# Kernel tuning notes

Measured on AMD Instinct MI355X. Metric: run time of the kernel, lower is better.

## Reference

```python
import jax, jax.numpy as jnp
import numpy as np

CONSOLIDATION_RATE = 0.001
FORGETTING_RATE = 0.0001
INITIAL_CONSOLIDATION_TIME = 100
WEIGHT_DIM = (4096, 4096)


def setup_inputs() -> dict:
    key = jax.random.key(0)
    ks = jax.random.split(key, 8)
    return {
        "current_weights": jax.random.normal(ks[0], WEIGHT_DIM, dtype=jnp.float32) * 0.1,
        "weight_changes": jax.random.normal(ks[1], WEIGHT_DIM, dtype=jnp.float32) * 0.01,
        # update_rule: Linear(3,16) -> ReLU -> Linear(16,1) -> Tanh
        "ur_w1": jax.random.normal(ks[2], (16, 3), dtype=jnp.float32) * 0.5,
        "ur_b1": jnp.zeros((16,), dtype=jnp.float32),
        "ur_w2": jax.random.normal(ks[3], (1, 16), dtype=jnp.float32) * 0.3,
        "ur_b2": jnp.zeros((1,), dtype=jnp.float32),
        # forgetting_gater: Linear(2,8) -> ReLU -> Linear(8,1) -> Sigmoid
        "fg_w1": jax.random.normal(ks[4], (8, 2), dtype=jnp.float32) * 0.5,
        "fg_b1": jnp.zeros((8,), dtype=jnp.float32),
        "fg_w2": jax.random.normal(ks[5], (1, 8), dtype=jnp.float32) * 0.3,
        "fg_b2": jnp.zeros((1,), dtype=jnp.float32),
    }


def reference(current_weights, weight_changes, ur_w1, ur_b1, ur_w2, ur_b2,
              fg_w1, fg_b1, fg_w2, fg_b2):
    # --- consolidation strength (first call: history len == 1, so strength = base) ---
    base_strength = jax.nn.sigmoid(jnp.linalg.norm(current_weights))
    final_strength = jnp.clip(base_strength, 0.0, 1.0)
    change_magnitude = jnp.linalg.norm(weight_changes)  # reported only

    # --- forgetting gate: input [time_factor, forgetting_rate] ---
    time_factor = min(1.0 / INITIAL_CONSOLIDATION_TIME, 1.0)  # 0.01 (python const)
    fx = jnp.array([time_factor, FORGETTING_RATE], dtype=current_weights.dtype)
    fh = jax.nn.relu(fx @ fg_w1.T + fg_b1)                 # [8]
    forgetting_strength = jax.nn.sigmoid(fh @ fg_w2.T + fg_b2)[0]  # scalar

    # --- consolidation dynamics: tiny 3->16->1 MLP vectorized over all N elements ---
    flat = current_weights.reshape(-1)                      # [N]
    # inputs per element are (w_i, final_strength, forgetting_strength); the last two
    # are scalars, so fold them into a per-hidden-unit bias instead of building [N,3].
    hidden_bias = final_strength * ur_w1[:, 1] + forgetting_strength * ur_w1[:, 2] + ur_b1  # [16]
    h = jax.nn.relu(flat[:, None] * ur_w1[:, 0] + hidden_bias)  # [N,16]
    update = jnp.tanh(h @ ur_w2[0] + ur_b2[0]) * CONSOLIDATION_RATE  # [N]
    new_weights = jnp.clip(flat + update, -10.0, 10.0).reshape(current_weights.shape)

    # --- quality / stability / memory strength (first-call values) ---
    weight_stability = jnp.asarray(0.5, dtype=current_weights.dtype)  # history < 10
    mean_abs = jnp.mean(jnp.abs(new_weights))
    dist_quality = jnp.where((mean_abs > 0.1) & (mean_abs < 0.9), 1.0, mean_abs)
    consolidation_quality = (weight_stability + dist_quality) / 2.0
    memory_strength = jnp.asarray(0.0, dtype=current_weights.dtype)   # history < 5

    return (new_weights, final_strength, change_magnitude, forgetting_strength,
            consolidation_quality, weight_stability, memory_strength)
```

## Files before the change

### kernel.cpp

```cpp
#include <hip/hip_runtime.h>
#include <math.h>

typedef float vfloat4 __attribute__((ext_vector_type(4)));
typedef float vfloat2 __attribute__((ext_vector_type(2)));

#define UNROLL 8
#define NBLK 2048
#define THREADS 256


__global__ __launch_bounds__(256) void wc_reduce_w(const vfloat4* __restrict__ w,
                                                   float* __restrict__ w_part,
                                                   int n4) {
    int tid = blockIdx.x * blockDim.x + threadIdx.x;
    int stride = gridDim.x * blockDim.x;
    float s0 = 0.f, s1 = 0.f, s2 = 0.f, s3 = 0.f;
    int i = tid;
    for (; i + (UNROLL - 1) * stride < n4; i += UNROLL * stride) {
        vfloat4 a[UNROLL];
#pragma unroll
        for (int u = 0; u < UNROLL; u++) a[u] = w[i + u * stride];
#pragma unroll
        for (int u = 0; u < UNROLL; u++) {
            s0 = fmaf(a[u].x, a[u].x, s0);
            s1 = fmaf(a[u].y, a[u].y, s1);
            s2 = fmaf(a[u].z, a[u].z, s2);
            s3 = fmaf(a[u].w, a[u].w, s3);
        }
    }
    for (; i < n4; i += stride) {
        vfloat4 a = w[i];
        s0 = fmaf(a.x, a.x, s0); s1 = fmaf(a.y, a.y, s1);
        s2 = fmaf(a.z, a.z, s2); s3 = fmaf(a.w, a.w, s3);
    }
    float sw = (s0 + s1) + (s2 + s3);
    for (int off = 32; off > 0; off >>= 1) sw += __shfl_down(sw, off);
    __shared__ float ls[4];
    int wave = threadIdx.x >> 6;
    int lane = threadIdx.x & 63;
    if (lane == 0) ls[wave] = sw;
    __syncthreads();
    if (threadIdx.x == 0)
        w_part[blockIdx.x] = (ls[0] + ls[1]) + (ls[2] + ls[3]);
}

__global__ __launch_bounds__(1024) void wc_scalars(const float* __restrict__ w_part,
                                                   float* __restrict__ wsf,
                                                   const float* __restrict__ fg_w1,
                                                   const float* __restrict__ fg_b1,
                                                   const float* __restrict__ fg_w2,
                                                   const float* __restrict__ fg_b2,
                                                   float* __restrict__ out_tail) {
    double sw = 0.0;
    for (int i = threadIdx.x; i < NBLK; i += 1024) sw += (double)w_part[i];
    for (int off = 32; off > 0; off >>= 1) sw += __shfl_down(sw, off);
    __shared__ double lsw[16];
    int wave = threadIdx.x >> 6;
    int lane = threadIdx.x & 63;
    if (lane == 0) lsw[wave] = sw;
    __syncthreads();
    if (threadIdx.x == 0) {
        double tw = 0.0;
        for (int k = 0; k < 16; k++) tw += lsw[k];
        float normw = sqrtf((float)tw);
        float fs = 1.0f / (1.0f + expf(-normw));
        fs = fminf(fmaxf(fs, 0.0f), 1.0f);
        const float tf = 0.01f, fr = 0.0001f;
        float acc = fg_b2[0];
        for (int j = 0; j < 8; j++) {
            float h = tf * fg_w1[2 * j + 0] + fr * fg_w1[2 * j + 1] + fg_b1[j];
            acc = fmaf(fmaxf(h, 0.0f), fg_w2[j], acc);
        }
        float fg = 1.0f / (1.0f + expf(-acc));
        wsf[0] = fs;
        wsf[1] = fg;
        out_tail[0] = fs;
        out_tail[2] = fg;
        out_tail[4] = 0.5f;
        out_tail[5] = 0.0f;
    }
}

__global__ __launch_bounds__(256) void wc_consolidate(const vfloat4* __restrict__ w,
                                                      const vfloat4* __restrict__ dw,
                                                      vfloat4* __restrict__ outw,
                                                      const float* __restrict__ ur_w1,
                                                      const float* __restrict__ ur_b1,
                                                      const float* __restrict__ ur_w2,
                                                      const float* __restrict__ ur_b2,
                                                      const float* __restrict__ wsf,
                                                      vfloat2* __restrict__ cd_part,
                                                      int n4) {
    float fs = wsf[0];
    float fg = wsf[1];
    float a0[16], hb[16], w2[16];
#pragma unroll
    for (int k = 0; k < 16; k++) {
        a0[k] = ur_w1[3 * k + 0];
        hb[k] = fmaf(fs, ur_w1[3 * k + 1], fmaf(fg, ur_w1[3 * k + 2], ur_b1[k]));
        w2[k] = ur_w2[k];
    }
    float b2 = ur_b2[0];

    int tid = blockIdx.x * blockDim.x + threadIdx.x;
    int stride = gridDim.x * blockDim.x;
    float sabs = 0.f;
    vfloat2 sdv01 = {0.f, 0.f}, sdv23 = {0.f, 0.f};
    int i = tid;
    for (; i + (UNROLL - 1) * stride < n4; i += UNROLL * stride) {
        vfloat4 v[UNROLL], d[UNROLL];
#pragma unroll
        for (int u = 0; u < UNROLL; u++) v[u] = w[i + u * stride];
#pragma unroll
        for (int u = 0; u < UNROLL; u++) d[u] = dw[i + u * stride];
#pragma unroll
        for (int u = 0; u < UNROLL; u++) {
            vfloat2 d01 = {d[u].x, d[u].y}, d23 = {d[u].z, d[u].w};
            sdv01 += d01 * d01;
            sdv23 += d23 * d23;
            vfloat2 x01 = {v[u].x, v[u].y}, x23 = {v[u].z, v[u].w};
            vfloat2 acc01 = {b2, b2}, acc23 = {b2, b2};
#pragma unroll
            for (int k = 0; k < 16; k++) {
                vfloat2 h01 = x01 * a0[k] + hb[k];
                vfloat2 h23 = x23 * a0[k] + hb[k];
                h01 = __builtin_elementwise_max(h01, (vfloat2)0.0f);
                h23 = __builtin_elementwise_max(h23, (vfloat2)0.0f);
                acc01 += h01 * w2[k];
                acc23 += h23 * w2[k];
            }
            float accs[4] = {acc01.x, acc01.y, acc23.x, acc23.y};
            float xs[4] = {v[u].x, v[u].y, v[u].z, v[u].w};
            vfloat4 o;
#pragma unroll
            for (int e = 0; e < 4; e++) {
                float t = __expf(2.0f * accs[e]);
                float th = fmaf(-2.0f, __builtin_amdgcn_rcpf(t + 1.0f), 1.0f);
                float nw = fmaf(0.001f, th, xs[e]);
                nw = fminf(fmaxf(nw, -10.0f), 10.0f);
                o[e] = nw;
                sabs += fabsf(nw);
            }
            outw[i + u * stride] = o;
        }
    }
    for (; i < n4; i += stride) {
        vfloat4 v = w[i];
        vfloat4 d = dw[i];
        vfloat2 d01 = {d.x, d.y}, d23 = {d.z, d.w};
        sdv01 += d01 * d01;
        sdv23 += d23 * d23;
        vfloat4 o;
#pragma unroll
        for (int e = 0; e < 4; e++) {
            float x = v[e];
            float acc = b2;
#pragma unroll
            for (int k = 0; k < 16; k++) {
                float h = fmaf(x, a0[k], hb[k]);
                acc = fmaf(fmaxf(h, 0.0f), w2[k], acc);
            }
            float t = __expf(2.0f * acc);
            float th = fmaf(-2.0f, __builtin_amdgcn_rcpf(t + 1.0f), 1.0f);
            float nw = fmaf(0.001f, th, x);
            nw = fminf(fmaxf(nw, -10.0f), 10.0f);
            o[e] = nw;
            sabs += fabsf(nw);
        }
        outw[i] = o;
    }
    float sdw = (sdv01.x + sdv01.y) + (sdv23.x + sdv23.y);
    for (int off = 32; off > 0; off >>= 1) {
        sabs += __shfl_down(sabs, off);
        sdw  += __shfl_down(sdw, off);
    }
    __shared__ float lsa[4], lsd[4];
    int wave = threadIdx.x >> 6;
    int lane = threadIdx.x & 63;
    if (lane == 0) { lsa[wave] = sabs; lsd[wave] = sdw; }
    __syncthreads();
    if (threadIdx.x == 0) {
        vfloat2 p;
        p.x = (lsa[0] + lsa[1]) + (lsa[2] + lsa[3]);
        p.y = (lsd[0] + lsd[1]) + (lsd[2] + lsd[3]);
        cd_part[blockIdx.x] = p;
    }
}

__global__ __launch_bounds__(1024) void wc_finalize(const vfloat2* __restrict__ cd_part,
                                                    float* __restrict__ out_tail,
                                                    double inv_n) {
    double sa = 0.0, sd = 0.0;
    for (int i = threadIdx.x; i < NBLK; i += 1024) {
        vfloat2 p = cd_part[i];
        sa += (double)p.x;
        sd += (double)p.y;
    }
    for (int off = 32; off > 0; off >>= 1) {
        sa += __shfl_down(sa, off);
        sd += __shfl_down(sd, off);
    }
    __shared__ double lsa[16], lsd[16];
    int wave = threadIdx.x >> 6;
    int lane = threadIdx.x & 63;
    if (lane == 0) { lsa[wave] = sa; lsd[wave] = sd; }
    __syncthreads();
    if (threadIdx.x == 0) {
        double ta = 0.0, td = 0.0;
        for (int k = 0; k < 16; k++) { ta += lsa[k]; td += lsd[k]; }
        out_tail[1] = sqrtf((float)td);
        float mean_abs = (float)(ta * inv_n);
        float dq = (mean_abs > 0.1f && mean_abs < 0.9f) ? 1.0f : mean_abs;
        out_tail[3] = (0.5f + dq) * 0.5f;
    }
}

extern "C" void kernel_launch(void* const* d_in, const int* in_sizes, int n_in,
                              void* d_out, int out_size, void* d_ws, size_t ws_size,
                              hipStream_t stream) {
    const float* cur_w = (const float*)d_in[0];
    const float* w_chg = (const float*)d_in[1];
    const float* ur_w1 = (const float*)d_in[2];
    const float* ur_b1 = (const float*)d_in[3];
    const float* ur_w2 = (const float*)d_in[4];
    const float* ur_b2 = (const float*)d_in[5];
    const float* fg_w1 = (const float*)d_in[6];
    const float* fg_b1 = (const float*)d_in[7];
    const float* fg_w2 = (const float*)d_in[8];
    const float* fg_b2 = (const float*)d_in[9];

    int n = in_sizes[0];
    int n4 = n / 4;

    float* w_part = (float*)d_ws;
    vfloat2* cd_part = (vfloat2*)((char*)d_ws + 8192);
    float* wsf = (float*)((char*)d_ws + 24576);

    float* out_w = (float*)d_out;
    float* out_tail = out_w + n;

    wc_reduce_w<<<NBLK, THREADS, 0, stream>>>((const vfloat4*)cur_w, w_part, n4);

    wc_scalars<<<1, 1024, 0, stream>>>(w_part, wsf, fg_w1, fg_b1, fg_w2, fg_b2, out_tail);

    wc_consolidate<<<NBLK, THREADS, 0, stream>>>((const vfloat4*)cur_w, (const vfloat4*)w_chg,
                                                 (vfloat4*)out_w, ur_w1, ur_b1, ur_w2, ur_b2,
                                                 wsf, cd_part, n4);

    wc_finalize<<<1, 1024, 0, stream>>>(cd_part, out_tail, 1.0 / (double)n);
}
```

Measured before the change: 202.9 us.

## Fold scalar kernel into consolidate pass and shrink norm reduction grid

Removes the single-block scalar kernel by having every consolidate block re-reduce the 512 norm partials and compute the sigmoid and forgetting-gate scalars itself. This cuts one launch and its serialization point. The first pass now uses 512 blocks instead of 2048. The main loop becomes a single-iteration if, which assumes the grid exactly covers the data with UNROLL; otherwise the tail loop handles the rest. Each block now redundantly reads the partials, and the partial-sum layout is split into two arrays.

```diff
diff --git a/kernel.cpp b/kernel.cpp
--- a/kernel.cpp
+++ b/kernel.cpp
@@ -5,13 +5,14 @@
 typedef float vfloat2 __attribute__((ext_vector_type(2)));
 
 #define UNROLL 8
+#define NBLK1 512
 #define NBLK 2048
 #define THREADS 256
 
 
-__global__ __launch_bounds__(256) void wc_reduce_w(const vfloat4* __restrict__ w,
-                                                   float* __restrict__ w_part,
-                                                   int n4) {
+__global__ __launch_bounds__(256) void wc_pass1(const vfloat4* __restrict__ w,
+                                                float* __restrict__ w_part,
+                                                int n4) {
     int tid = blockIdx.x * blockDim.x + threadIdx.x;
     int stride = gridDim.x * blockDim.x;
     float s0 = 0.f, s1 = 0.f, s2 = 0.f, s3 = 0.f;
@@ -44,55 +45,56 @@
         w_part[blockIdx.x] = (ls[0] + ls[1]) + (ls[2] + ls[3]);
 }
 
-__global__ __launch_bounds__(1024) void wc_scalars(const float* __restrict__ w_part,
-                                                   float* __restrict__ wsf,
-                                                   const float* __restrict__ fg_w1,
-                                                   const float* __restrict__ fg_b1,
-                                                   const float* __restrict__ fg_w2,
-                                                   const float* __restrict__ fg_b2,
-                                                   float* __restrict__ out_tail) {
-    double sw = 0.0;
-    for (int i = threadIdx.x; i < NBLK; i += 1024) sw += (double)w_part[i];
-    for (int off = 32; off > 0; off >>= 1) sw += __shfl_down(sw, off);
-    __shared__ double lsw[16];
+__global__ __launch_bounds__(256) void wc_pass2(const vfloat4* __restrict__ w,
+                                                const vfloat4* __restrict__ dw,
+                                                vfloat4* __restrict__ outw,
+                                                const float* __restrict__ ur_w1,
+                                                const float* __restrict__ ur_b1,
+                                                const float* __restrict__ ur_w2,
+                                                const float* __restrict__ ur_b2,
+                                                const float* __restrict__ fg_w1,
+                                                const float* __restrict__ fg_b1,
+                                                const float* __restrict__ fg_w2,
+                                                const float* __restrict__ fg_b2,
+                                                const float* __restrict__ w_part,
+                                                float* __restrict__ sa_part,
+                                                float* __restrict__ sd_part,
+                                                float* __restrict__ out_tail,
+                                                int n4) {
     int wave = threadIdx.x >> 6;
     int lane = threadIdx.x & 63;
-    if (lane == 0) lsw[wave] = sw;
+
+    double pw = 0.0;
+    for (int k = threadIdx.x; k < NBLK1; k += THREADS) pw += (double)w_part[k];
+    for (int off = 32; off > 0; off >>= 1) pw += __shfl_down(pw, off);
+    __shared__ double lspw[4];
+    __shared__ float s_fs, s_fg;
+    if (lane == 0) lspw[wave] = pw;
     __syncthreads();
     if (threadIdx.x == 0) {
-        double tw = 0.0;
-        for (int k = 0; k < 16; k++) tw += lsw[k];
+        double tw = (lspw[0] + lspw[1]) + (lspw[2] + lspw[3]);
         float normw = sqrtf((float)tw);
-        float fs = 1.0f / (1.0f + expf(-normw));
-        fs = fminf(fmaxf(fs, 0.0f), 1.0f);
+        float fsv = 1.0f / (1.0f + expf(-normw));
+        fsv = fminf(fmaxf(fsv, 0.0f), 1.0f);
         const float tf = 0.01f, fr = 0.0001f;
         float acc = fg_b2[0];
         for (int j = 0; j < 8; j++) {
             float h = tf * fg_w1[2 * j + 0] + fr * fg_w1[2 * j + 1] + fg_b1[j];
             acc = fmaf(fmaxf(h, 0.0f), fg_w2[j], acc);
         }
-        float fg = 1.0f / (1.0f + expf(-acc));
-        wsf[0] = fs;
-        wsf[1] = fg;
-        out_tail[0] = fs;
-        out_tail[2] = fg;
-        out_tail[4] = 0.5f;
-        out_tail[5] = 0.0f;
-    }
-}
-
-__global__ __launch_bounds__(256) void wc_consolidate(const vfloat4* __restrict__ w,
-                                                      const vfloat4* __restrict__ dw,
-                                                      vfloat4* __restrict__ outw,
-                                                      const float* __restrict__ ur_w1,
-                                                      const float* __restrict__ ur_b1,
-                                                      const float* __restrict__ ur_w2,
-                                                      const float* __restrict__ ur_b2,
-                                                      const float* __restrict__ wsf,
-                                                      vfloat2* __restrict__ cd_part,
-                                                      int n4) {
-    float fs = wsf[0];
-    float fg = wsf[1];
+        s_fs = fsv;
+        s_fg = 1.0f / (1.0f + expf(-acc));
+        if (blockIdx.x == 0) {
+            out_tail[0] = fsv;
+            out_tail[2] = s_fg;
+            out_tail[4] = 0.5f;
+            out_tail[5] = 0.0f;
+        }
+    }
+    __syncthreads();
+    float fs = s_fs;
+    float fg = s_fg;
+
     float a0[16], hb[16], w2[16];
 #pragma unroll
     for (int k = 0; k < 16; k++) {
@@ -107,7 +109,7 @@
     float sabs = 0.f;
     vfloat2 sdv01 = {0.f, 0.f}, sdv23 = {0.f, 0.f};
     int i = tid;
-    for (; i + (UNROLL - 1) * stride < n4; i += UNROLL * stride) {
+    if (i + (UNROLL - 1) * stride < n4) {
         vfloat4 v[UNROLL], d[UNROLL];
 #pragma unroll
         for (int u = 0; u < UNROLL; u++) v[u] = w[i + u * stride];
@@ -143,6 +145,7 @@
             }
             outw[i + u * stride] = o;
         }
+        i += UNROLL * stride;
     }
     for (; i < n4; i += stride) {
         vfloat4 v = w[i];
@@ -169,32 +172,29 @@
         }
         outw[i] = o;
     }
+
     float sdw = (sdv01.x + sdv01.y) + (sdv23.x + sdv23.y);
     for (int off = 32; off > 0; off >>= 1) {
         sabs += __shfl_down(sabs, off);
         sdw  += __shfl_down(sdw, off);
     }
     __shared__ float lsa[4], lsd[4];
-    int wave = threadIdx.x >> 6;
-    int lane = threadIdx.x & 63;
     if (lane == 0) { lsa[wave] = sabs; lsd[wave] = sdw; }
     __syncthreads();
     if (threadIdx.x == 0) {
-        vfloat2 p;
-        p.x = (lsa[0] + lsa[1]) + (lsa[2] + lsa[3]);
-        p.y = (lsd[0] + lsd[1]) + (lsd[2] + lsd[3]);
-        cd_part[blockIdx.x] = p;
-    }
-}
-
-__global__ __launch_bounds__(1024) void wc_finalize(const vfloat2* __restrict__ cd_part,
-                                                    float* __restrict__ out_tail,
-                                                    double inv_n) {
+        sa_part[blockIdx.x] = (lsa[0] + lsa[1]) + (lsa[2] + lsa[3]);
+        sd_part[blockIdx.x] = (lsd[0] + lsd[1]) + (lsd[2] + lsd[3]);
+    }
+}
+
+__global__ __launch_bounds__(1024) void wc_pass3(const float* __restrict__ sa_part,
+                                                 const float* __restrict__ sd_part,
+                                                 float* __restrict__ out_tail,
+                                                 double inv_n) {
     double sa = 0.0, sd = 0.0;
     for (int i = threadIdx.x; i < NBLK; i += 1024) {
-        vfloat2 p = cd_part[i];
-        sa += (double)p.x;
-        sd += (double)p.y;
+        sa += (double)sa_part[i];
+        sd += (double)sd_part[i];
     }
     for (int off = 32; off > 0; off >>= 1) {
         sa += __shfl_down(sa, off);
@@ -233,19 +233,18 @@
     int n4 = n / 4;
 
     float* w_part = (float*)d_ws;
-    vfloat2* cd_part = (vfloat2*)((char*)d_ws + 8192);
-    float* wsf = (float*)((char*)d_ws + 24576);
+    float* sa_part = (float*)((char*)d_ws + 8192);
+    float* sd_part = (float*)((char*)d_ws + 16384);
 
     float* out_w = (float*)d_out;
     float* out_tail = out_w + n;
 
-    wc_reduce_w<<<NBLK, THREADS, 0, stream>>>((const vfloat4*)cur_w, w_part, n4);
-
-    wc_scalars<<<1, 1024, 0, stream>>>(w_part, wsf, fg_w1, fg_b1, fg_w2, fg_b2, out_tail);
-
-    wc_consolidate<<<NBLK, THREADS, 0, stream>>>((const vfloat4*)cur_w, (const vfloat4*)w_chg,
-                                                 (vfloat4*)out_w, ur_w1, ur_b1, ur_w2, ur_b2,
-                                                 wsf, cd_part, n4);
-
-    wc_finalize<<<1, 1024, 0, stream>>>(cd_part, out_tail, 1.0 / (double)n);
-}
+    wc_pass1<<<NBLK1, THREADS, 0, stream>>>((const vfloat4*)cur_w, w_part, n4);
+
+    wc_pass2<<<NBLK, THREADS, 0, stream>>>((const vfloat4*)cur_w, (const vfloat4*)w_chg,
+                                           (vfloat4*)out_w, ur_w1, ur_b1, ur_w2, ur_b2,
+                                           fg_w1, fg_b1, fg_w2, fg_b2,
+                                           w_part, sa_part, sd_part, out_tail, n4);
+
+    wc_pass3<<<1, 1024, 0, stream>>>(sa_part, sd_part, out_tail, 1.0 / (double)n);
+}
```

New measurement: 207.5 us. 1.02x slower.
